# Kernel optimization log

Hardware: AMD Instinct MI355X
Metric: run time of the kernel (lower is better)

The kernel has to match this reference:

```python
import jax, jax.numpy as jnp
import numpy as np

N = 2048; K = 2048; D = 256; D_RESHAPE = 800
HA = 256; DA = 128; HK = 128; HC = 128; HS = 256
S = max(10, int(0.1 * K))  # n_sample = 204
BN_SCALE = 1.0 / float(np.sqrt(1.0 + 1e-5))  # eval BatchNorm1d with running stats (0,1)

def leaky(x):
    return jax.nn.leaky_relu(x, 0.01)

def conv2d(x, w, b):
    y = jax.lax.conv_general_dilated(x, w, (1, 1), 'VALID', dimension_numbers=('NCHW', 'OIHW', 'NCHW'))
    return y + b[None, :, None, None]

def maxpool2(x):
    return jax.lax.reduce_window(x, -jnp.inf, jax.lax.max, (1, 1, 2, 2), (1, 1, 2, 2), 'VALID')

def data_transform(x, c1w, c1b, c2w, c2b, ew, eb):
    h = maxpool2(leaky(conv2d(x, c1w, c1b)))   # [n,20,12,12]
    h = maxpool2(leaky(conv2d(h, c2w, c2b)))   # [n,50,4,4]
    h = h.reshape(-1, D_RESHAPE)
    return leaky(h @ ew.T + eb)                # [n,D]

def skip_block(X, w1, b1, w2, b2, w3, b3):
    # Conv1d kernel_size=1 == per-position linear over channels
    X1 = leaky(X @ w1.T + b1) * BN_SCALE       # [n,HC]
    X2 = leaky(X @ w2.T + b2) * BN_SCALE       # [n,HC]
    X3 = leaky(X @ w3.T + b3) * BN_SCALE       # [n,d]
    feat = jax.nn.softmax(X1 @ X2.T, axis=0)   # torch Softmax(dim=1) on [1,n,n] -> axis 0
    return feat @ X3 + X

def mask_scores(A, w1, b1, w2, b2, w3, b3, w4, b4):
    X1 = leaky(A @ w1.T + b1)                  # [n,HK]
    X2 = jnp.tanh(A @ w2.T + b2)               # [n,HK]
    M = X1.T @ X2                              # [HK,HK]
    A3 = leaky(M @ w3.T + b3)                  # [HK,K]
    s = A3.T @ w4[0] + b4[0]                   # [K]
    return jax.nn.softmax(s)

def attention(X, few, feb, vw, vb, uw, ub, aww, awb, ew, eb):
    H = leaky(X @ few.T + feb)                 # [n,HA]
    AV = jnp.tanh(H @ vw.T + vb)
    AU = leaky(H @ uw.T + ub)
    a = leaky((AV * AU) @ aww.T + awb)         # [n,1]
    A = jax.nn.softmax(a.T, axis=1)            # [1,n]
    M = leaky((A @ H) @ ew.T + eb)             # [1,d]
    return M, A

def euclid(X, Y):
    d2 = jnp.sum(X * X, 1)[:, None] + jnp.sum(Y * Y, 1)[None, :] - 2.0 * (X @ Y.T)
    return jnp.sqrt(jnp.maximum(d2, 0.0))


def setup_inputs() -> dict:
    key = jax.random.key(0)
    ks = iter(jax.random.split(key, 70))
    def rn(shape, scale=0.05):
        return jax.random.normal(next(ks), shape, dtype=jnp.float32) * scale
    d = {}
    d['B'] = jax.random.normal(next(ks), (N, 1, 28, 28), dtype=jnp.float32)
    d['KB'] = jax.random.normal(next(ks), (K, 1, 28, 28), dtype=jnp.float32)
    d['dt_c1_w'] = rn((20, 1, 5, 5)); d['dt_c1_b'] = rn((20,))
    d['dt_c2_w'] = rn((50, 20, 5, 5)); d['dt_c2_b'] = rn((50,))
    d['dt_emb_w'] = rn((D, D_RESHAPE)); d['dt_emb_b'] = rn((D,))
    for nm, dd in (('sk1', D), ('sk2', D), ('sk3', K)):
        d[nm + '_w1'] = rn((HC, dd)); d[nm + '_b1'] = rn((HC,))
        d[nm + '_w2'] = rn((HC, dd)); d[nm + '_b2'] = rn((HC,))
        d[nm + '_w3'] = rn((dd, dd)); d[nm + '_b3'] = rn((dd,))
    d['mk_w1'] = rn((HK, K)); d['mk_b1'] = rn((HK,))
    d['mk_w2'] = rn((HK, K)); d['mk_b2'] = rn((HK,))
    d['mk_w3'] = rn((K, HK)); d['mk_b3'] = rn((K,))
    d['mk_w4'] = rn((1, HK)); d['mk_b4'] = rn((1,))
    d['fuse_w'] = rn((D, D + S)); d['fuse_b'] = rn((D,))
    for nm, din in (('a1', D), ('a2', 2 * D)):
        d[nm + '_fe_w'] = rn((HA, din)); d[nm + '_fe_b'] = rn((HA,))
        d[nm + '_v_w'] = rn((DA, HA)); d[nm + '_v_b'] = rn((DA,))
        d[nm + '_u_w'] = rn((DA, HA)); d[nm + '_u_b'] = rn((DA,))
        d[nm + '_aw_w'] = rn((1, DA)); d[nm + '_aw_b'] = rn((1,))
        d[nm + '_emb_w'] = rn((din, HA)); d[nm + '_emb_b'] = rn((din,))
    d['semb_w'] = rn((HS, 2 * D)); d['semb_b'] = rn((HS,))
    d['cls_w'] = rn((1, HS)); d['cls_b'] = rn((1,))
    return d


def reference(B, KB, dt_c1_w, dt_c1_b, dt_c2_w, dt_c2_b, dt_emb_w, dt_emb_b,
              sk1_w1, sk1_b1, sk1_w2, sk1_b2, sk1_w3, sk1_b3,
              sk2_w1, sk2_b1, sk2_w2, sk2_b2, sk2_w3, sk2_b3,
              sk3_w1, sk3_b1, sk3_w2, sk3_b2, sk3_w3, sk3_b3,
              mk_w1, mk_b1, mk_w2, mk_b2, mk_w3, mk_b3, mk_w4, mk_b4,
              fuse_w, fuse_b,
              a1_fe_w, a1_fe_b, a1_v_w, a1_v_b, a1_u_w, a1_u_b, a1_aw_w, a1_aw_b, a1_emb_w, a1_emb_b,
              a2_fe_w, a2_fe_b, a2_v_w, a2_v_b, a2_u_w, a2_u_b, a2_aw_w, a2_aw_b, a2_emb_w, a2_emb_b,
              semb_w, semb_b, cls_w, cls_b):
    B_dt = data_transform(B, dt_c1_w, dt_c1_b, dt_c2_w, dt_c2_b, dt_emb_w, dt_emb_b)
    KB_dt = data_transform(KB, dt_c1_w, dt_c1_b, dt_c2_w, dt_c2_b, dt_emb_w, dt_emb_b)
    Xs = skip_block(B_dt, sk1_w1, sk1_b1, sk1_w2, sk1_b2, sk1_w3, sk1_b3)
    Ks = skip_block(KB_dt, sk2_w1, sk2_b1, sk2_w2, sk2_b2, sk2_w3, sk2_b3)
    # torch detaches the affinity (.detach().numpy())
    aff = euclid(jax.lax.stop_gradient(Xs), jax.lax.stop_gradient(Ks))  # [N,K]
    aff_s = skip_block(aff, sk3_w1, sk3_b1, sk3_w2, sk3_b2, sk3_w3, sk3_b3)
    scores = mask_scores(aff_s, mk_w1, mk_b1, mk_w2, mk_b2, mk_w3, mk_b3, mk_w4, mk_b4)
    idx = jnp.argsort(-scores)[:S]                       # top-S knowledge columns
    B_bag = jax.nn.softmax(aff_s[:, idx], axis=1)        # [N,S], torch Softmax(dim=2)
    B_fuse = leaky(jnp.concatenate([B_dt, B_bag], axis=1) @ fuse_w.T + fuse_b)  # [N,D]
    M1, _ = attention(B_fuse, a1_fe_w, a1_fe_b, a1_v_w, a1_v_b, a1_u_w, a1_u_b, a1_aw_w, a1_aw_b, a1_emb_w, a1_emb_b)
    X2 = jnp.concatenate([B_fuse, jnp.tile(M1, (B_fuse.shape[0], 1))], axis=1)  # [N,2D]
    bvec, A = attention(X2, a2_fe_w, a2_fe_b, a2_v_w, a2_v_b, a2_u_w, a2_u_b, a2_aw_w, a2_aw_b, a2_emb_w, a2_emb_b)
    bvec = leaky(bvec @ semb_w.T + semb_b)               # [1,HS]
    Y = jnp.clip(jax.nn.sigmoid(bvec @ cls_w.T + cls_b), 1e-5, 1.0 - 1e-5)
    return (Y, A)
```

## Files before the change

kernel.cpp:

```cpp
#include <hip/hip_runtime.h>
#include <math.h>

#define LEAKY(x) ((x) > 0.f ? (x) : 0.01f * (x))
static constexpr float BN_SCALE = 0.9999950000374997f;

typedef unsigned short ushort_t;
typedef float f32x4 __attribute__((ext_vector_type(4)));
typedef short bf16x8 __attribute__((ext_vector_type(8)));

__device__ __forceinline__ ushort_t f2bfu(float f) {
  union { float f; unsigned u; } v; v.f = f;
  unsigned r = v.u + 0x7fffu + ((v.u >> 16) & 1u);
  return (ushort_t)(r >> 16);
}
__device__ __forceinline__ float bfu2f(ushort_t u) {
  union { unsigned u; float f; } v; v.u = ((unsigned)u) << 16;
  return v.f;
}

__global__ void fill_out(float* out, int n) {
  int i = blockIdx.x * 256 + threadIdx.x;
  if (i < n) out[i] = 0.25f;
}

struct CvtArgs {
  const float* src[20];
  ushort_t* dst[20];
  int len[20];
};
__global__ void to_bf16_multi(CvtArgs a) {
  for (int s = 0; s < 20; ++s) {
    const float* sp = a.src[s];
    ushort_t* dp = a.dst[s];
    int n = a.len[s];
    for (int i = blockIdx.x * 256 + threadIdx.x; i < n; i += gridDim.x * 256)
      dp[i] = f2bfu(sp[i]);
  }
}

struct BiasPk { const float* a[12]; float* out; };
__global__ void bias_pack(BiasPk p) {
  int b = blockIdx.x, t = threadIdx.x;
  p.out[b * 256 + t] = (t < 128) ? p.a[2 * b][t] : p.a[2 * b + 1][t - 128];
}

__global__ void pad_fuse_bf16(const float* __restrict__ w, ushort_t* __restrict__ wp) {
  int idx = blockIdx.x * 256 + threadIdx.x;
  if (idx >= 256 * 512) return;
  int o = idx >> 9, k = idx & 511;
  wp[idx] = (k < 460) ? f2bfu(w[(size_t)o * 460 + k]) : (ushort_t)0;
}

__launch_bounds__(256)
__global__ void conv12_mfma(const float* __restrict__ imgB, const float* __restrict__ imgK,
                            const float* __restrict__ w1, const float* __restrict__ b1,
                            const ushort_t* __restrict__ w2b, const float* __restrict__ b2,
                            ushort_t* __restrict__ out800) {
  __shared__ __align__(16) char smem[39168];
  ushort_t* sh1u = (ushort_t*)smem;
  float* simg = (float*)(smem + 11520);
  float* sw1p = (float*)(smem + 18688);
  float* b1s  = (float*)(smem + 20928);
  ushort_t* As = (ushort_t*)(smem + 11520);
  ushort_t* Bs = (ushort_t*)(smem + 29952);
  float* Cf = (float*)smem;

  int tid = threadIdx.x;
  int bx = blockIdx.x;
  const float* imgb = (bx < 1024) ? imgB + (size_t)bx * 2 * 784
                                  : imgK + (size_t)(bx - 1024) * 2 * 784;

  for (int i = tid; i < 1568; i += 256) {
    int im = (i >= 784) ? 1 : 0;
    int r = i - im * 784;
    int row = r / 28, col = r - row * 28;
    int sc = col ^ ((((unsigned)row >> 1) & 1u) << 4);
    simg[im * 896 + row * 32 + sc] = imgb[i];
  }
  for (int i = tid; i < 500; i += 256) {
    int c = i / 25, tap = i - c * 25;
    sw1p[c * 28 + tap] = w1[i];
  }
  if (tid < 20) b1s[tid] = b1[tid];
  __syncthreads();

  for (int o = tid; o < 1152; o += 256) {
    int im = (o >= 576) ? 1 : 0;
    int rem = o - im * 576;
    int cg = rem / 144;
    int pos = rem - cg * 144;
    int py = pos / 12, px = pos - py * 12;
    int y0 = py * 2, x0 = px * 2;
    float p[6][6];
    #pragma unroll
    for (int yy = 0; yy < 6; ++yy) {
      int rr = y0 + yy;
      int rbase = im * 896 + rr * 32;
      int sw = (((unsigned)rr >> 1) & 1u) << 4;
      #pragma unroll
      for (int xx = 0; xx < 6; ++xx)
        p[yy][xx] = simg[rbase + ((x0 + xx) ^ sw)];
    }
    #pragma unroll
    for (int cc = 0; cc < 5; ++cc) {
      int c = cg * 5 + cc;
      float wreg[28];
      const float* wc = &sw1p[c * 28];
      #pragma unroll
      for (int q = 0; q < 7; ++q)
        *(f32x4*)&wreg[4 * q] = *(const f32x4*)(wc + 4 * q);
      float bb = b1s[c];
      float t0 = bb, t1 = bb, t2 = bb, t3 = bb;
      #pragma unroll
      for (int ky = 0; ky < 5; ++ky)
        #pragma unroll
        for (int kx = 0; kx < 5; ++kx) {
          float wv = wreg[ky * 5 + kx];
          t0 += p[ky][kx] * wv;
          t1 += p[ky][kx + 1] * wv;
          t2 += p[ky + 1][kx] * wv;
          t3 += p[ky + 1][kx + 1] * wv;
        }
      float mx = fmaxf(fmaxf(t0, t1), fmaxf(t2, t3));
      sh1u[im * 2880 + c * 144 + pos] = f2bfu(LEAKY(mx));
    }
  }

  int wave = tid >> 6, lane = tid & 63;
  int wm = (wave >> 1) * 64, wn = (wave & 1) * 32;
  int mrow = lane & 15, kq = lane >> 4;
  int kl = tid & 63, rbase = tid >> 6;

  f32x4 acc[4][2];
  #pragma unroll
  for (int i = 0; i < 4; ++i)
    #pragma unroll
    for (int j = 0; j < 2; ++j)
      #pragma unroll
      for (int r = 0; r < 4; ++r) acc[i][j][r] = 0.f;

  for (int k0 = 0; k0 < 512; k0 += 64) {
    __syncthreads();
    int k = k0 + kl;
    bool valid = k < 500;
    int ic = k / 25, tap = k - ic * 25;
    int ky = tap / 5, kx = tap - ky * 5;
    int kof = ic * 144 + ky * 12 + kx;
    ushort_t tA[32];
    #pragma unroll
    for (int i = 0; i < 32; ++i) {
      int r = rbase + 4 * i;
      int im = r >> 6, pos = r & 63, oy = pos >> 3, ox = pos & 7;
      tA[i] = valid ? sh1u[im * 2880 + kof + oy * 12 + ox] : (ushort_t)0;
    }
    ushort_t tB[16];
    #pragma unroll
    for (int i = 0; i < 16; ++i) {
      int oc = rbase + 4 * i;
      tB[i] = (valid && oc < 50) ? w2b[(size_t)oc * 500 + k] : (ushort_t)0;
    }
    #pragma unroll
    for (int i = 0; i < 32; ++i) As[(rbase + 4 * i) * 72 + kl] = tA[i];
    #pragma unroll
    for (int i = 0; i < 16; ++i) Bs[(rbase + 4 * i) * 72 + kl] = tB[i];
    __syncthreads();
    #pragma unroll
    for (int ks = 0; ks < 2; ++ks) {
      bf16x8 af[4], bf[2];
      #pragma unroll
      for (int mt = 0; mt < 4; ++mt)
        af[mt] = *(const bf16x8*)&As[(wm + mt * 16 + mrow) * 72 + ks * 32 + kq * 8];
      #pragma unroll
      for (int nt = 0; nt < 2; ++nt)
        bf[nt] = *(const bf16x8*)&Bs[(wn + nt * 16 + mrow) * 72 + ks * 32 + kq * 8];
      #pragma unroll
      for (int mt = 0; mt < 4; ++mt)
        #pragma unroll
        for (int nt = 0; nt < 2; ++nt)
          acc[mt][nt] = __builtin_amdgcn_mfma_f32_16x16x32_bf16(af[mt], bf[nt], acc[mt][nt], 0, 0, 0);
    }
  }
  __syncthreads();
  #pragma unroll
  for (int mt = 0; mt < 4; ++mt)
    #pragma unroll
    for (int nt = 0; nt < 2; ++nt) {
      int n0 = wn + nt * 16 + (lane & 15);
      #pragma unroll
      for (int r = 0; r < 4; ++r)
        Cf[(wm + mt * 16 + kq * 4 + r) * 68 + n0] = acc[mt][nt][r];
    }
  __syncthreads();
  for (int o = tid; o < 1600; o += 256) {
    int im = o / 800, oi = o - im * 800;
    int oc = oi >> 4, p = oi & 15, py = p >> 2, px = p & 3;
    int r0 = im * 64 + py * 16 + px * 2;
    float bb = b2[oc];
    float t0 = LEAKY(Cf[r0 * 68 + oc] + bb);
    float t1 = LEAKY(Cf[(r0 + 1) * 68 + oc] + bb);
    float t2 = LEAKY(Cf[(r0 + 8) * 68 + oc] + bb);
    float t3 = LEAKY(Cf[(r0 + 9) * 68 + oc] + bb);
    out800[(size_t)(bx * 2 + im) * 800 + oi] = f2bfu(fmaxf(fmaxf(t0, t1), fmaxf(t2, t3)));
  }
}

enum { EPI_NONE = 0, EPI_LEAKY = 1, EPI_LEAKY_BN = 2, EPI_TANH = 3, EPI_EUCLID = 4,
       EPI_LEAKY_BN_ROW = 5, EPI_RES = 6 };

#define LROW 40

template <int EPI>
__launch_bounds__(256)
__global__ void gemm_bf16_nt(const ushort_t* __restrict__ A, const ushort_t* __restrict__ B,
                             const float* __restrict__ bias, float* __restrict__ C32,
                             ushort_t* __restrict__ C16, int M, int N, int Kd,
                             const float* __restrict__ e1, const float* __restrict__ e2) {
  __shared__ ushort_t As[128 * LROW];
  __shared__ ushort_t Bs[128 * LROW];
  int tid = threadIdx.x;
  int bm = blockIdx.y * 128, bn = blockIdx.x * 128;
  int wave = tid >> 6, lane = tid & 63;
  int wm = (wave >> 1) * 64, wn = (wave & 1) * 64;
  int mrow = lane & 15, kq = lane >> 4;
  int srow = tid >> 1, skof = (tid & 1) * 16;

  f32x4 acc[4][4];
  #pragma unroll
  for (int i = 0; i < 4; ++i)
    #pragma unroll
    for (int j = 0; j < 4; ++j)
      #pragma unroll
      for (int r = 0; r < 4; ++r) acc[i][j][r] = 0.f;

  for (int k0 = 0; k0 < Kd; k0 += 32) {
    const uint4* ap = (const uint4*)(A + (size_t)(bm + srow) * Kd + k0 + skof);
    const uint4* bp = (const uint4*)(B + (size_t)(bn + srow) * Kd + k0 + skof);
    uint4 a0 = ap[0], a1 = ap[1];
    uint4 b0 = bp[0], b1 = bp[1];
    __syncthreads();
    *(uint4*)&As[srow * LROW + skof] = a0;
    *(uint4*)&As[srow * LROW + skof + 8] = a1;
    *(uint4*)&Bs[srow * LROW + skof] = b0;
    *(uint4*)&Bs[srow * LROW + skof + 8] = b1;
    __syncthreads();
    bf16x8 af[4], bf[4];
    #pragma unroll
    for (int mt = 0; mt < 4; ++mt)
      af[mt] = *(const bf16x8*)&As[(wm + mt * 16 + mrow) * LROW + kq * 8];
    #pragma unroll
    for (int nt = 0; nt < 4; ++nt)
      bf[nt] = *(const bf16x8*)&Bs[(wn + nt * 16 + mrow) * LROW + kq * 8];
    #pragma unroll
    for (int mt = 0; mt < 4; ++mt)
      #pragma unroll
      for (int nt = 0; nt < 4; ++nt)
        acc[mt][nt] = __builtin_amdgcn_mfma_f32_16x16x32_bf16(af[mt], bf[nt], acc[mt][nt], 0, 0, 0);
  }
  #pragma unroll
  for (int mt = 0; mt < 4; ++mt)
    #pragma unroll
    for (int nt = 0; nt < 4; ++nt) {
      int n_g = bn + wn + nt * 16 + (lane & 15);
      #pragma unroll
      for (int r = 0; r < 4; ++r) {
        int m_g = bm + wm + mt * 16 + kq * 4 + r;
        float v = acc[mt][nt][r];
        if (EPI == EPI_EUCLID) {
          v = e1[m_g] + e2[n_g] - 2.f * v;
          v = sqrtf(fmaxf(v, 0.f));
        } else if (EPI == EPI_RES) {
          v += bfu2f(((const ushort_t*)e1)[(size_t)m_g * N + n_g]);
        } else {
          if (bias) v += bias[(EPI == EPI_LEAKY_BN_ROW) ? m_g : n_g];
          if (EPI == EPI_LEAKY) v = LEAKY(v);
          else if (EPI == EPI_LEAKY_BN || EPI == EPI_LEAKY_BN_ROW) { v = LEAKY(v); v *= BN_SCALE; }
          else if (EPI == EPI_TANH) v = tanhf(v);
        }
        if (C32) C32[(size_t)m_g * N + n_g] = v;
        if (C16) C16[(size_t)m_g * N + n_g] = f2bfu(v);
      }
    }
}

__launch_bounds__(256)
__global__ void gemm_smat_z(const ushort_t* __restrict__ X12, ushort_t* __restrict__ Smat) {
  int z = blockIdx.z;
  const ushort_t* A = X12 + (size_t)z * 2048 * 256;
  const ushort_t* B = A + 128;
  ushort_t* C = Smat + (size_t)z * 2048 * 2048;
  __shared__ ushort_t As[128 * LROW];
  __shared__ ushort_t Bs[128 * LROW];
  int tid = threadIdx.x;
  int bm = blockIdx.y * 128, bn = blockIdx.x * 128;
  int wave = tid >> 6, lane = tid & 63;
  int wm = (wave >> 1) * 64, wn = (wave & 1) * 64;
  int mrow = lane & 15, kq = lane >> 4;
  int srow = tid >> 1, skof = (tid & 1) * 16;

  f32x4 acc[4][4];
  #pragma unroll
  for (int i = 0; i < 4; ++i)
    #pragma unroll
    for (int j = 0; j < 4; ++j)
      #pragma unroll
      for (int r = 0; r < 4; ++r) acc[i][j][r] = 0.f;

  for (int k0 = 0; k0 < 128; k0 += 32) {
    const uint4* ap = (const uint4*)(A + (size_t)(bm + srow) * 256 + k0 + skof);
    const uint4* bp = (const uint4*)(B + (size_t)(bn + srow) * 256 + k0 + skof);
    uint4 a0 = ap[0], a1 = ap[1];
    uint4 b0 = bp[0], b1 = bp[1];
    __syncthreads();
    *(uint4*)&As[srow * LROW + skof] = a0;
    *(uint4*)&As[srow * LROW + skof + 8] = a1;
    *(uint4*)&Bs[srow * LROW + skof] = b0;
    *(uint4*)&Bs[srow * LROW + skof + 8] = b1;
    __syncthreads();
    bf16x8 af[4], bf[4];
    #pragma unroll
    for (int mt = 0; mt < 4; ++mt)
      af[mt] = *(const bf16x8*)&As[(wm + mt * 16 + mrow) * LROW + kq * 8];
    #pragma unroll
    for (int nt = 0; nt < 4; ++nt)
      bf[nt] = *(const bf16x8*)&Bs[(wn + nt * 16 + mrow) * LROW + kq * 8];
    #pragma unroll
    for (int mt = 0; mt < 4; ++mt)
      #pragma unroll
      for (int nt = 0; nt < 4; ++nt)
        acc[mt][nt] = __builtin_amdgcn_mfma_f32_16x16x32_bf16(af[mt], bf[nt], acc[mt][nt], 0, 0, 0);
  }
  #pragma unroll
  for (int mt = 0; mt < 4; ++mt)
    #pragma unroll
    for (int nt = 0; nt < 4; ++nt) {
      int n_g = bn + wn + nt * 16 + (lane & 15);
      #pragma unroll
      for (int r = 0; r < 4; ++r) {
        int m_g = bm + wm + mt * 16 + kq * 4 + r;
        C[(size_t)m_g * 2048 + n_g] = f2bfu(acc[mt][nt][r]);
      }
    }
}

template <int EPI>
__launch_bounds__(256)
__global__ void gemm_bf16_nt64(const ushort_t* __restrict__ A, const ushort_t* __restrict__ B,
                               const float* __restrict__ bias, float* __restrict__ C32,
                               ushort_t* __restrict__ C16, int M, int N, int Kd) {
  __shared__ ushort_t As[64 * LROW];
  __shared__ ushort_t Bs[64 * LROW];
  int tid = threadIdx.x;
  int bm = blockIdx.y * 64, bn = blockIdx.x * 64;
  int wave = tid >> 6, lane = tid & 63;
  int wm = (wave >> 1) * 32, wn = (wave & 1) * 32;
  int mrow = lane & 15, kq = lane >> 4;
  int srow = tid >> 2, skof = (tid & 3) * 8;

  f32x4 acc[2][2];
  #pragma unroll
  for (int i = 0; i < 2; ++i)
    #pragma unroll
    for (int j = 0; j < 2; ++j)
      #pragma unroll
      for (int r = 0; r < 4; ++r) acc[i][j][r] = 0.f;

  for (int k0 = 0; k0 < Kd; k0 += 32) {
    uint4 a0 = *(const uint4*)(A + (size_t)(bm + srow) * Kd + k0 + skof);
    uint4 b0 = *(const uint4*)(B + (size_t)(bn + srow) * Kd + k0 + skof);
    __syncthreads();
    *(uint4*)&As[srow * LROW + skof] = a0;
    *(uint4*)&Bs[srow * LROW + skof] = b0;
    __syncthreads();
    bf16x8 af[2], bf[2];
    #pragma unroll
    for (int mt = 0; mt < 2; ++mt)
      af[mt] = *(const bf16x8*)&As[(wm + mt * 16 + mrow) * LROW + kq * 8];
    #pragma unroll
    for (int nt = 0; nt < 2; ++nt)
      bf[nt] = *(const bf16x8*)&Bs[(wn + nt * 16 + mrow) * LROW + kq * 8];
    #pragma unroll
    for (int mt = 0; mt < 2; ++mt)
      #pragma unroll
      for (int nt = 0; nt < 2; ++nt)
        acc[mt][nt] = __builtin_amdgcn_mfma_f32_16x16x32_bf16(af[mt], bf[nt], acc[mt][nt], 0, 0, 0);
  }
  #pragma unroll
  for (int mt = 0; mt < 2; ++mt)
    #pragma unroll
    for (int nt = 0; nt < 2; ++nt) {
      int n_g = bn + wn + nt * 16 + (lane & 15);
      #pragma unroll
      for (int r = 0; r < 4; ++r) {
        int m_g = bm + wm + mt * 16 + kq * 4 + r;
        float v = acc[mt][nt][r];
        if (bias) v += bias[n_g];
        if (EPI == EPI_LEAKY) v = LEAKY(v);
        else if (EPI == EPI_LEAKY_BN) { v = LEAKY(v); v *= BN_SCALE; }
        else if (EPI == EPI_TANH) v = tanhf(v);
        if (C32) C32[(size_t)m_g * N + n_g] = v;
        if (C16) C16[(size_t)m_g * N + n_g] = f2bfu(v);
      }
    }
}

template <int EPI>
__launch_bounds__(256)
__global__ void gemm_nt64_dual(const ushort_t* __restrict__ A, const ushort_t* __restrict__ B1,
                               const ushort_t* __restrict__ B2, const float* __restrict__ bias1,
                               const float* __restrict__ bias2, ushort_t* __restrict__ C16,
                               int M, int N, int Kd, int Msplit) {
  __shared__ ushort_t As[64 * LROW];
  __shared__ ushort_t Bs[64 * LROW];
  int tid = threadIdx.x;
  int bm = blockIdx.y * 64, bn = blockIdx.x * 64;
  const ushort_t* B = (bm < Msplit) ? B1 : B2;
  const float* bias = (bm < Msplit) ? bias1 : bias2;
  int wave = tid >> 6, lane = tid & 63;
  int wm = (wave >> 1) * 32, wn = (wave & 1) * 32;
  int mrow = lane & 15, kq = lane >> 4;
  int srow = tid >> 2, skof = (tid & 3) * 8;

  f32x4 acc[2][2];
  #pragma unroll
  for (int i = 0; i < 2; ++i)
    #pragma unroll
    for (int j = 0; j < 2; ++j)
      #pragma unroll
      for (int r = 0; r < 4; ++r) acc[i][j][r] = 0.f;

  for (int k0 = 0; k0 < Kd; k0 += 32) {
    uint4 a0 = *(const uint4*)(A + (size_t)(bm + srow) * Kd + k0 + skof);
    uint4 b0 = *(const uint4*)(B + (size_t)(bn + srow) * Kd + k0 + skof);
    __syncthreads();
    *(uint4*)&As[srow * LROW + skof] = a0;
    *(uint4*)&Bs[srow * LROW + skof] = b0;
    __syncthreads();
    bf16x8 af[2], bf[2];
    #pragma unroll
    for (int mt = 0; mt < 2; ++mt)
      af[mt] = *(const bf16x8*)&As[(wm + mt * 16 + mrow) * LROW + kq * 8];
    #pragma unroll
    for (int nt = 0; nt < 2; ++nt)
      bf[nt] = *(const bf16x8*)&Bs[(wn + nt * 16 + mrow) * LROW + kq * 8];
    #pragma unroll
    for (int mt = 0; mt < 2; ++mt)
      #pragma unroll
      for (int nt = 0; nt < 2; ++nt)
        acc[mt][nt] = __builtin_amdgcn_mfma_f32_16x16x32_bf16(af[mt], bf[nt], acc[mt][nt], 0, 0, 0);
  }
  #pragma unroll
  for (int mt = 0; mt < 2; ++mt)
    #pragma unroll
    for (int nt = 0; nt < 2; ++nt) {
      int n_g = bn + wn + nt * 16 + (lane & 15);
      #pragma unroll
      for (int r = 0; r < 4; ++r) {
        int m_g = bm + wm + mt * 16 + kq * 4 + r;
        float v = acc[mt][nt][r] + bias[n_g];
        if (EPI == EPI_LEAKY) v = LEAKY(v);
        else if (EPI == EPI_LEAKY_BN) { v = LEAKY(v); v *= BN_SCALE; }
        C16[(size_t)m_g * N + n_g] = f2bfu(v);
      }
    }
}

template <int EPI1, int EPI2>
__launch_bounds__(256)
__global__ void gemm_nt64_split(const ushort_t* __restrict__ A, const ushort_t* __restrict__ B,
                                const float* __restrict__ biasPk, float* __restrict__ C32,
                                ushort_t* __restrict__ C16, int M, int N, int Kd, int Nsplit) {
  __shared__ ushort_t As[64 * LROW];
  __shared__ ushort_t Bs[64 * LROW];
  int tid = threadIdx.x;
  int bm = blockIdx.y * 64, bn = blockIdx.x * 64;
  int wave = tid >> 6, lane = tid & 63;
  int wm = (wave >> 1) * 32, wn = (wave & 1) * 32;
  int mrow = lane & 15, kq = lane >> 4;
  int srow = tid >> 2, skof = (tid & 3) * 8;

  f32x4 acc[2][2];
  #pragma unroll
  for (int i = 0; i < 2; ++i)
    #pragma unroll
    for (int j = 0; j < 2; ++j)
      #pragma unroll
      for (int r = 0; r < 4; ++r) acc[i][j][r] = 0.f;

  for (int k0 = 0; k0 < Kd; k0 += 32) {
    uint4 a0 = *(const uint4*)(A + (size_t)(bm + srow) * Kd + k0 + skof);
    uint4 b0 = *(const uint4*)(B + (size_t)(bn + srow) * Kd + k0 + skof);
    __syncthreads();
    *(uint4*)&As[srow * LROW + skof] = a0;
    *(uint4*)&Bs[srow * LROW + skof] = b0;
    __syncthreads();
    bf16x8 af[2], bf[2];
    #pragma unroll
    for (int mt = 0; mt < 2; ++mt)
      af[mt] = *(const bf16x8*)&As[(wm + mt * 16 + mrow) * LROW + kq * 8];
    #pragma unroll
    for (int nt = 0; nt < 2; ++nt)
      bf[nt] = *(const bf16x8*)&Bs[(wn + nt * 16 + mrow) * LROW + kq * 8];
    #pragma unroll
    for (int mt = 0; mt < 2; ++mt)
      #pragma unroll
      for (int nt = 0; nt < 2; ++nt)
        acc[mt][nt] = __builtin_amdgcn_mfma_f32_16x16x32_bf16(af[mt], bf[nt], acc[mt][nt], 0, 0, 0);
  }
  #pragma unroll
  for (int mt = 0; mt < 2; ++mt)
    #pragma unroll
    for (int nt = 0; nt < 2; ++nt) {
      int n_g = bn + wn + nt * 16 + (lane & 15);
      #pragma unroll
      for (int r = 0; r < 4; ++r) {
        int m_g = bm + wm + mt * 16 + kq * 4 + r;
        float v = acc[mt][nt][r] + biasPk[n_g];
        if (n_g < Nsplit) {
          if (EPI1 == EPI_LEAKY) v = LEAKY(v);
          else if (EPI1 == EPI_TANH) v = tanhf(v);
        } else {
          if (EPI2 == EPI_LEAKY) v = LEAKY(v);
          else if (EPI2 == EPI_TANH) v = tanhf(v);
        }
        if (C32) C32[(size_t)m_g * N + n_g] = v;
        if (C16) C16[(size_t)m_g * N + n_g] = f2bfu(v);
      }
    }
}

__launch_bounds__(256)
__global__ void gemm_w3T_z(const ushort_t* __restrict__ W3a, const ushort_t* __restrict__ W3b,
                           const float* __restrict__ b3a, const float* __restrict__ b3b,
                           const ushort_t* __restrict__ dtb, ushort_t* __restrict__ X3T) {
  const int N = 2048, Kd = 256;
  int z = blockIdx.z;
  const ushort_t* A = z ? W3b : W3a;
  const float* bias = z ? b3b : b3a;
  const ushort_t* B = dtb + (size_t)z * 2048 * 256;
  ushort_t* C = X3T + (size_t)z * 256 * 2048;
  __shared__ ushort_t As[64 * LROW];
  __shared__ ushort_t Bs[64 * LROW];
  int tid = threadIdx.x;
  int bm = blockIdx.y * 64, bn = blockIdx.x * 64;
  int wave = tid >> 6, lane = tid & 63;
  int wm = (wave >> 1) * 32, wn = (wave & 1) * 32;
  int mrow = lane & 15, kq = lane >> 4;
  int srow = tid >> 2, skof = (tid & 3) * 8;

  f32x4 acc[2][2];
  #pragma unroll
  for (int i = 0; i < 2; ++i)
    #pragma unroll
    for (int j = 0; j < 2; ++j)
      #pragma unroll
      for (int r = 0; r < 4; ++r) acc[i][j][r] = 0.f;

  for (int k0 = 0; k0 < Kd; k0 += 32) {
    uint4 a0 = *(const uint4*)(A + (size_t)(bm + srow) * Kd + k0 + skof);
    uint4 b0 = *(const uint4*)(B + (size_t)(bn + srow) * Kd + k0 + skof);
    __syncthreads();
    *(uint4*)&As[srow * LROW + skof] = a0;
    *(uint4*)&Bs[srow * LROW + skof] = b0;
    __syncthreads();
    bf16x8 af[2], bf[2];
    #pragma unroll
    for (int mt = 0; mt < 2; ++mt)
      af[mt] = *(const bf16x8*)&As[(wm + mt * 16 + mrow) * LROW + kq * 8];
    #pragma unroll
    for (int nt = 0; nt < 2; ++nt)
      bf[nt] = *(const bf16x8*)&Bs[(wn + nt * 16 + mrow) * LROW + kq * 8];
    #pragma unroll
    for (int mt = 0; mt < 2; ++mt)
      #pragma unroll
      for (int nt = 0; nt < 2; ++nt)
        acc[mt][nt] = __builtin_amdgcn_mfma_f32_16x16x32_bf16(af[mt], bf[nt], acc[mt][nt], 0, 0, 0);
  }
  #pragma unroll
  for (int mt = 0; mt < 2; ++mt)
    #pragma unroll
    for (int nt = 0; nt < 2; ++nt) {
      int n_g = bn + wn + nt * 16 + (lane & 15);
      #pragma unroll
      for (int r = 0; r < 4; ++r) {
        int m_g = bm + wm + mt * 16 + kq * 4 + r;
        float v = acc[mt][nt][r] + bias[m_g];
        v = LEAKY(v); v *= BN_SCALE;
        C[(size_t)m_g * N + n_g] = f2bfu(v);
      }
    }
}

__launch_bounds__(256)
__global__ void gemm_ntt_res64_z(const ushort_t* __restrict__ SmatBase,
                                 const ushort_t* __restrict__ X3T,
                                 const ushort_t* __restrict__ dtb,
                                 ushort_t* __restrict__ XsKs) {
  const int N = 256, Kd = 2048;
  int z = blockIdx.z;
  const ushort_t* A = SmatBase + (size_t)z * 2048 * 2048;
  const ushort_t* B = X3T + (size_t)z * 256 * 2048;
  const ushort_t* R = dtb + (size_t)z * 2048 * 256;
  ushort_t* C = XsKs + (size_t)z * 2048 * 256;
  __shared__ ushort_t As[64 * LROW];
  __shared__ ushort_t Bs[64 * LROW];
  int tid = threadIdx.x;
  int bm = blockIdx.y * 64, bn = blockIdx.x * 64;
  int wave = tid >> 6, lane = tid & 63;
  int wm = (wave >> 1) * 32, wn = (wave & 1) * 32;
  int mrow = lane & 15, kq = lane >> 4;
  int srow = tid >> 2, skof = (tid & 3) * 8;

  f32x4 acc[2][2];
  #pragma unroll
  for (int i = 0; i < 2; ++i)
    #pragma unroll
    for (int j = 0; j < 2; ++j)
      #pragma unroll
      for (int r = 0; r < 4; ++r) acc[i][j][r] = 0.f;

  for (int k0 = 0; k0 < Kd; k0 += 32) {
    uint4 a0 = *(const uint4*)(A + (size_t)(bm + srow) * Kd + k0 + skof);
    uint4 b0 = *(const uint4*)(B + (size_t)(bn + srow) * Kd + k0 + skof);
    __syncthreads();
    *(uint4*)&As[srow * LROW + skof] = a0;
    *(uint4*)&Bs[srow * LROW + skof] = b0;
    __syncthreads();
    bf16x8 af[2], bf[2];
    #pragma unroll
    for (int mt = 0; mt < 2; ++mt)
      af[mt] = *(const bf16x8*)&As[(wm + mt * 16 + mrow) * LROW + kq * 8];
    #pragma unroll
    for (int nt = 0; nt < 2; ++nt)
      bf[nt] = *(const bf16x8*)&Bs[(wn + nt * 16 + mrow) * LROW + kq * 8];
    #pragma unroll
    for (int mt = 0; mt < 2; ++mt)
      #pragma unroll
      for (int nt = 0; nt < 2; ++nt)
        acc[mt][nt] = __builtin_amdgcn_mfma_f32_16x16x32_bf16(af[mt], bf[nt], acc[mt][nt], 0, 0, 0);
  }
  #pragma unroll
  for (int mt = 0; mt < 2; ++mt)
    #pragma unroll
    for (int nt = 0; nt < 2; ++nt) {
      int n_g = bn + wn + nt * 16 + (lane & 15);
      #pragma unroll
      for (int r = 0; r < 4; ++r) {
        int m_g = bm + wm + mt * 16 + kq * 4 + r;
        float v = acc[mt][nt][r] + bfu2f(R[(size_t)m_g * N + n_g]);
        C[(size_t)m_g * N + n_g] = f2bfu(v);
      }
    }
}

__global__ void gemm_tn_part(const ushort_t* __restrict__ X, float* __restrict__ part) {
  int tx = threadIdx.x & 15, ty = threadIdx.x >> 4;
  int i = blockIdx.y * 16 + ty, j = blockIdx.x * 16 + tx;
  int ks = blockIdx.z;
  float acc = 0.f;
  for (int k = ks * 128; k < ks * 128 + 128; ++k)
    acc += bfu2f(X[(size_t)k * 256 + i]) * bfu2f(X[(size_t)k * 256 + 128 + j]);
  part[(size_t)ks * 16384 + i * 128 + j] = acc;
}
__global__ void gemm_tn_reduce(const float* __restrict__ part, ushort_t* __restrict__ Mm) {
  int idx = blockIdx.x * 256 + threadIdx.x;
  float s = 0.f;
  #pragma unroll
  for (int ks = 0; ks < 16; ++ks) s += part[(size_t)ks * 16384 + idx];
  Mm[idx] = f2bfu(s);
}

__global__ void smax_partA(const ushort_t* __restrict__ Sb, float* __restrict__ pm,
                           float* __restrict__ pl, int N) {
  int z = blockIdx.z;
  const ushort_t* S = Sb + (size_t)z * 2048 * 2048;
  int t = threadIdx.x;
  int col = blockIdx.x * 64 + (t & 63);
  int g = t >> 6;
  int r0 = blockIdx.y * 128 + g;
  float vals[32];
  #pragma unroll
  for (int i = 0; i < 32; ++i)
    vals[i] = bfu2f(S[(size_t)(r0 + 4 * i) * N + col]);
  float m = -1e30f;
  #pragma unroll
  for (int i = 0; i < 32; ++i) m = fmaxf(m, vals[i]);
  float l = 0.f;
  #pragma unroll
  for (int i = 0; i < 32; ++i) l += expf(vals[i] - m);
  __shared__ float rm[4][64], rl[4][64];
  rm[g][t & 63] = m; rl[g][t & 63] = l;
  __syncthreads();
  if (g == 0) {
    int c = t & 63;
    float M0 = rm[0][c], L0 = rl[0][c];
    #pragma unroll
    for (int j = 1; j < 4; ++j) {
      float Mj = rm[j][c], Lj = rl[j][c];
      float nm = fmaxf(M0, Mj);
      L0 = L0 * expf(M0 - nm) + Lj * expf(Mj - nm);
      M0 = nm;
    }
    pm[((size_t)z * 16 + blockIdx.y) * N + col] = M0;
    pl[((size_t)z * 16 + blockIdx.y) * N + col] = L0;
  }
}
__global__ void smax_partB(const float* __restrict__ pm, const float* __restrict__ pl,
                           float* __restrict__ gm, float* __restrict__ gi, int N) {
  int z = blockIdx.y;
  int col = blockIdx.x * 256 + threadIdx.x;
  float m = -1e30f, l = 0.f;
  for (int b = 0; b < 16; ++b) {
    float bm = pm[((size_t)z * 16 + b) * N + col], bl = pl[((size_t)z * 16 + b) * N + col];
    float nm = fmaxf(m, bm);
    l = l * expf(m - nm) + bl * expf(bm - nm);
    m = nm;
  }
  gm[(size_t)z * N + col] = m;
  gi[(size_t)z * N + col] = 1.f / l;
}
__global__ void smax_partC(ushort_t* __restrict__ Sb, const float* __restrict__ gm,
                           const float* __restrict__ gi, int N) {
  int z = blockIdx.z;
  ushort_t* S = Sb + (size_t)z * 2048 * 2048;
  int t = threadIdx.x;
  int col = blockIdx.x * 64 + (t & 63);
  int g = t >> 6;
  float m = gm[(size_t)z * N + col], inv = gi[(size_t)z * N + col];
  int r0 = blockIdx.y * 128 + g;
  #pragma unroll 8
  for (int i = 0; i < 32; ++i) {
    size_t idx = (size_t)(r0 + 4 * i) * N + col;
    S[idx] = f2bfu(expf(bfu2f(S[idx]) - m) * inv);
  }
}

__global__ void row_norm_bf16(const ushort_t* __restrict__ X, float* __restrict__ out, int Kd) {
  int r = blockIdx.x;
  int t = threadIdx.x;
  float s = 0.f;
  for (int k = t; k < Kd; k += 64) { float v = bfu2f(X[(size_t)r * Kd + k]); s += v * v; }
  for (int off = 32; off; off >>= 1) s += __shfl_down(s, off);
  if (t == 0) out[r] = s;
}

__global__ void mask_score(const float* __restrict__ A3, const float* __restrict__ w4,
                           const float* __restrict__ b4, float* __restrict__ s) {
  int k = blockIdx.x * 256 + threadIdx.x;
  float acc = b4[0];
  for (int h = 0; h < 128; ++h) acc += A3[(size_t)h * 2048 + k] * w4[h];
  s[k] = acc;
}

__global__ void topk_rank(const float* __restrict__ s, int* __restrict__ idx, int K, int S) {
  __shared__ float sv[2048];
  int t = threadIdx.x;
  for (int i = t; i < K; i += 256) sv[i] = s[i];
  __syncthreads();
  int j = blockIdx.x * 256 + t;
  if (j >= K) return;
  float sj = sv[j];
  int rank = 0;
  #pragma unroll 8
  for (int i = 0; i < 2048; ++i) {
    float si = sv[i];
    rank += (si > sj) || (si == sj && i < j);
  }
  if (rank < S) idx[rank] = j;
}

__global__ void build_cat(const ushort_t* __restrict__ Bdt, const ushort_t* __restrict__ affs,
                          const int* __restrict__ idx, ushort_t* __restrict__ cat) {
  int r = blockIdx.x, t = threadIdx.x;
  __shared__ float vals[256];
  __shared__ float red[256];
  float v = -1e30f;
  if (t < 204) {
    int ix = idx[t];
    ix = ix < 0 ? 0 : (ix > 2047 ? 2047 : ix);
    v = bfu2f(affs[(size_t)r * 2048 + ix]);
  }
  vals[t] = v;
  red[t] = v;
  __syncthreads();
  for (int off = 128; off; off >>= 1) { if (t < off) red[t] = fmaxf(red[t], red[t + off]); __syncthreads(); }
  float m = red[0];
  __syncthreads();
// ... 270 lines not shown
```

Before: 922.5 us.

## Use direct global-to-LDS loads in all bf16 GEMM kernels, simplify conv1 staging

```diff
diff --git a/kernel.cpp b/kernel.cpp
--- a/kernel.cpp
+++ b/kernel.cpp
@@ -16,6 +16,12 @@
 __device__ __forceinline__ float bfu2f(ushort_t u) {
   union { unsigned u; float f; } v; v.u = ((unsigned)u) << 16;
   return v.f;
+}
+
+__device__ __forceinline__ void gload16(const ushort_t* g, ushort_t* lds) {
+  __builtin_amdgcn_global_load_lds(
+      (const __attribute__((address_space(1))) void*)g,
+      (__attribute__((address_space(3))) void*)lds, 16, 0, 0);
 }
 
 __global__ void fill_out(float* out, int n) {
@@ -59,7 +65,7 @@
   __shared__ __align__(16) char smem[39168];
   ushort_t* sh1u = (ushort_t*)smem;
   float* simg = (float*)(smem + 11520);
-  float* sw1p = (float*)(smem + 18688);
+  float* sw1  = (float*)(smem + 18688);
   float* b1s  = (float*)(smem + 20928);
   ushort_t* As = (ushort_t*)(smem + 11520);
   ushort_t* Bs = (ushort_t*)(smem + 29952);
@@ -74,13 +80,10 @@
     int im = (i >= 784) ? 1 : 0;
     int r = i - im * 784;
     int row = r / 28, col = r - row * 28;
-    int sc = col ^ ((((unsigned)row >> 1) & 1u) << 4);
+    int sc = (col + (row >> 1)) & 31;
     simg[im * 896 + row * 32 + sc] = imgb[i];
   }
-  for (int i = tid; i < 500; i += 256) {
-    int c = i / 25, tap = i - c * 25;
-    sw1p[c * 28 + tap] = w1[i];
-  }
+  for (int i = tid; i < 500; i += 256) sw1[i] = w1[i];
   if (tid < 20) b1s[tid] = b1[tid];
   __syncthreads();
 
@@ -96,26 +99,22 @@
     for (int yy = 0; yy < 6; ++yy) {
       int rr = y0 + yy;
       int rbase = im * 896 + rr * 32;
-      int sw = (((unsigned)rr >> 1) & 1u) << 4;
+      int rot = rr >> 1;
       #pragma unroll
       for (int xx = 0; xx < 6; ++xx)
-        p[yy][xx] = simg[rbase + ((x0 + xx) ^ sw)];
+        p[yy][xx] = simg[rbase + ((x0 + xx + rot) & 31)];
     }
     #pragma unroll
     for (int cc = 0; cc < 5; ++cc) {
       int c = cg * 5 + cc;
-      float wreg[28];
-      const float* wc = &sw1p[c * 28];
-      #pragma unroll
-      for (int q = 0; q < 7; ++q)
-        *(f32x4*)&wreg[4 * q] = *(const f32x4*)(wc + 4 * q);
+      const float* wc = &sw1[c * 25];
       float bb = b1s[c];
       float t0 = bb, t1 = bb, t2 = bb, t3 = bb;
       #pragma unroll
       for (int ky = 0; ky < 5; ++ky)
         #pragma unroll
         for (int kx = 0; kx < 5; ++kx) {
-          float wv = wreg[ky * 5 + kx];
+          float wv = wc[ky * 5 + kx];
           t0 += p[ky][kx] * wv;
           t1 += p[ky][kx + 1] * wv;
           t2 += p[ky + 1][kx] * wv;
@@ -215,14 +214,18 @@
                              const float* __restrict__ bias, float* __restrict__ C32,
                              ushort_t* __restrict__ C16, int M, int N, int Kd,
                              const float* __restrict__ e1, const float* __restrict__ e2) {
-  __shared__ ushort_t As[128 * LROW];
-  __shared__ ushort_t Bs[128 * LROW];
+  __shared__ __align__(16) ushort_t As[128 * 32];
+  __shared__ __align__(16) ushort_t Bs[128 * 32];
   int tid = threadIdx.x;
   int bm = blockIdx.y * 128, bn = blockIdx.x * 128;
   int wave = tid >> 6, lane = tid & 63;
   int wm = (wave >> 1) * 64, wn = (wave & 1) * 64;
   int mrow = lane & 15, kq = lane >> 4;
-  int srow = tid >> 1, skof = (tid & 1) * 16;
+  int l0 = tid, l1 = tid + 256;
+  const ushort_t* ga0 = A + (size_t)(bm + (l0 >> 2)) * Kd + (l0 & 3) * 8;
+  const ushort_t* ga1 = A + (size_t)(bm + (l1 >> 2)) * Kd + (l1 & 3) * 8;
+  const ushort_t* gb0 = B + (size_t)(bn + (l0 >> 2)) * Kd + (l0 & 3) * 8;
+  const ushort_t* gb1 = B + (size_t)(bn + (l1 >> 2)) * Kd + (l1 & 3) * 8;
 
   f32x4 acc[4][4];
   #pragma unroll
@@ -233,23 +236,19 @@
       for (int r = 0; r < 4; ++r) acc[i][j][r] = 0.f;
 
   for (int k0 = 0; k0 < Kd; k0 += 32) {
-    const uint4* ap = (const uint4*)(A + (size_t)(bm + srow) * Kd + k0 + skof);
-    const uint4* bp = (const uint4*)(B + (size_t)(bn + srow) * Kd + k0 + skof);
-    uint4 a0 = ap[0], a1 = ap[1];
-    uint4 b0 = bp[0], b1 = bp[1];
-    __syncthreads();
-    *(uint4*)&As[srow * LROW + skof] = a0;
-    *(uint4*)&As[srow * LROW + skof + 8] = a1;
-    *(uint4*)&Bs[srow * LROW + skof] = b0;
-    *(uint4*)&Bs[srow * LROW + skof + 8] = b1;
+    __syncthreads();
+    gload16(ga0 + k0, &As[l0 * 8]);
+    gload16(ga1 + k0, &As[l1 * 8]);
+    gload16(gb0 + k0, &Bs[l0 * 8]);
+    gload16(gb1 + k0, &Bs[l1 * 8]);
     __syncthreads();
     bf16x8 af[4], bf[4];
     #pragma unroll
     for (int mt = 0; mt < 4; ++mt)
-      af[mt] = *(const bf16x8*)&As[(wm + mt * 16 + mrow) * LROW + kq * 8];
+      af[mt] = *(const bf16x8*)&As[(wm + mt * 16 + mrow) * 32 + kq * 8];
     #pragma unroll
     for (int nt = 0; nt < 4; ++nt)
-      bf[nt] = *(const bf16x8*)&Bs[(wn + nt * 16 + mrow) * LROW + kq * 8];
+      bf[nt] = *(const bf16x8*)&Bs[(wn + nt * 16 + mrow) * 32 + kq * 8];
     #pragma unroll
     for (int mt = 0; mt < 4; ++mt)
       #pragma unroll
@@ -288,14 +287,18 @@
   const ushort_t* A = X12 + (size_t)z * 2048 * 256;
   const ushort_t* B = A + 128;
   ushort_t* C = Smat + (size_t)z * 2048 * 2048;
-  __shared__ ushort_t As[128 * LROW];
-  __shared__ ushort_t Bs[128 * LROW];
+  __shared__ __align__(16) ushort_t As[128 * 32];
+  __shared__ __align__(16) ushort_t Bs[128 * 32];
   int tid = threadIdx.x;
   int bm = blockIdx.y * 128, bn = blockIdx.x * 128;
   int wave = tid >> 6, lane = tid & 63;
   int wm = (wave >> 1) * 64, wn = (wave & 1) * 64;
   int mrow = lane & 15, kq = lane >> 4;
-  int srow = tid >> 1, skof = (tid & 1) * 16;
+  int l0 = tid, l1 = tid + 256;
+  const ushort_t* ga0 = A + (size_t)(bm + (l0 >> 2)) * 256 + (l0 & 3) * 8;
+  const ushort_t* ga1 = A + (size_t)(bm + (l1 >> 2)) * 256 + (l1 & 3) * 8;
+  const ushort_t* gb0 = B + (size_t)(bn + (l0 >> 2)) * 256 + (l0 & 3) * 8;
+  const ushort_t* gb1 = B + (size_t)(bn + (l1 >> 2)) * 256 + (l1 & 3) * 8;
 
   f32x4 acc[4][4];
   #pragma unroll
@@ -306,23 +309,19 @@
       for (int r = 0; r < 4; ++r) acc[i][j][r] = 0.f;
 
   for (int k0 = 0; k0 < 128; k0 += 32) {
-    const uint4* ap = (const uint4*)(A + (size_t)(bm + srow) * 256 + k0 + skof);
-    const uint4* bp = (const uint4*)(B + (size_t)(bn + srow) * 256 + k0 + skof);
-    uint4 a0 = ap[0], a1 = ap[1];
-    uint4 b0 = bp[0], b1 = bp[1];
-    __syncthreads();
-    *(uint4*)&As[srow * LROW + skof] = a0;
-    *(uint4*)&As[srow * LROW + skof + 8] = a1;
-    *(uint4*)&Bs[srow * LROW + skof] = b0;
-    *(uint4*)&Bs[srow * LROW + skof + 8] = b1;
+    __syncthreads();
+    gload16(ga0 + k0, &As[l0 * 8]);
+    gload16(ga1 + k0, &As[l1 * 8]);
+    gload16(gb0 + k0, &Bs[l0 * 8]);
+    gload16(gb1 + k0, &Bs[l1 * 8]);
     __syncthreads();
     bf16x8 af[4], bf[4];
     #pragma unroll
     for (int mt = 0; mt < 4; ++mt)
-      af[mt] = *(const bf16x8*)&As[(wm + mt * 16 + mrow) * LROW + kq * 8];
+      af[mt] = *(const bf16x8*)&As[(wm + mt * 16 + mrow) * 32 + kq * 8];
     #pragma unroll
     for (int nt = 0; nt < 4; ++nt)
-      bf[nt] = *(const bf16x8*)&Bs[(wn + nt * 16 + mrow) * LROW + kq * 8];
+      bf[nt] = *(const bf16x8*)&Bs[(wn + nt * 16 + mrow) * 32 + kq * 8];
     #pragma unroll
     for (int mt = 0; mt < 4; ++mt)
       #pragma unroll
@@ -347,14 +346,15 @@
 __global__ void gemm_bf16_nt64(const ushort_t* __restrict__ A, const ushort_t* __restrict__ B,
                                const float* __restrict__ bias, float* __restrict__ C32,
                                ushort_t* __restrict__ C16, int M, int N, int Kd) {
-  __shared__ ushort_t As[64 * LROW];
-  __shared__ ushort_t Bs[64 * LROW];
+  __shared__ __align__(16) ushort_t As[64 * 32];
+  __shared__ __align__(16) ushort_t Bs[64 * 32];
   int tid = threadIdx.x;
   int bm = blockIdx.y * 64, bn = blockIdx.x * 64;
   int wave = tid >> 6, lane = tid & 63;
   int wm = (wave >> 1) * 32, wn = (wave & 1) * 32;
   int mrow = lane & 15, kq = lane >> 4;
-  int srow = tid >> 2, skof = (tid & 3) * 8;
+  const ushort_t* ga = A + (size_t)(bm + (tid >> 2)) * Kd + (tid & 3) * 8;
+  const ushort_t* gb = B + (size_t)(bn + (tid >> 2)) * Kd + (tid & 3) * 8;
 
   f32x4 acc[2][2];
   #pragma unroll
@@ -365,19 +365,17 @@
       for (int r = 0; r < 4; ++r) acc[i][j][r] = 0.f;
 
   for (int k0 = 0; k0 < Kd; k0 += 32) {
-    uint4 a0 = *(const uint4*)(A + (size_t)(bm + srow) * Kd + k0 + skof);
-    uint4 b0 = *(const uint4*)(B + (size_t)(bn + srow) * Kd + k0 + skof);
-    __syncthreads();
-    *(uint4*)&As[srow * LROW + skof] = a0;
-    *(uint4*)&Bs[srow * LROW + skof] = b0;
+    __syncthreads();
+    gload16(ga + k0, &As[tid * 8]);
+    gload16(gb + k0, &Bs[tid * 8]);
     __syncthreads();
     bf16x8 af[2], bf[2];
     #pragma unroll
     for (int mt = 0; mt < 2; ++mt)
-      af[mt] = *(const bf16x8*)&As[(wm + mt * 16 + mrow) * LROW + kq * 8];
+      af[mt] = *(const bf16x8*)&As[(wm + mt * 16 + mrow) * 32 + kq * 8];
     #pragma unroll
     for (int nt = 0; nt < 2; ++nt)
-      bf[nt] = *(const bf16x8*)&Bs[(wn + nt * 16 + mrow) * LROW + kq * 8];
+      bf[nt] = *(const bf16x8*)&Bs[(wn + nt * 16 + mrow) * 32 + kq * 8];
     #pragma unroll
     for (int mt = 0; mt < 2; ++mt)
       #pragma unroll
@@ -409,8 +407,8 @@
                                const ushort_t* __restrict__ B2, const float* __restrict__ bias1,
                                const float* __restrict__ bias2, ushort_t* __restrict__ C16,
                                int M, int N, int Kd, int Msplit) {
-  __shared__ ushort_t As[64 * LROW];
-  __shared__ ushort_t Bs[64 * LROW];
+  __shared__ __align__(16) ushort_t As[64 * 32];
+  __shared__ __align__(16) ushort_t Bs[64 * 32];
   int tid = threadIdx.x;
   int bm = blockIdx.y * 64, bn = blockIdx.x * 64;
   const ushort_t* B = (bm < Msplit) ? B1 : B2;
@@ -418,7 +416,8 @@
   int wave = tid >> 6, lane = tid & 63;
   int wm = (wave >> 1) * 32, wn = (wave & 1) * 32;
   int mrow = lane & 15, kq = lane >> 4;
-  int srow = tid >> 2, skof = (tid & 3) * 8;
+  const ushort_t* ga = A + (size_t)(bm + (tid >> 2)) * Kd + (tid & 3) * 8;
+  const ushort_t* gb = B + (size_t)(bn + (tid >> 2)) * Kd + (tid & 3) * 8;
 
   f32x4 acc[2][2];
   #pragma unroll
@@ -429,19 +428,17 @@
       for (int r = 0; r < 4; ++r) acc[i][j][r] = 0.f;
 
   for (int k0 = 0; k0 < Kd; k0 += 32) {
-    uint4 a0 = *(const uint4*)(A + (size_t)(bm + srow) * Kd + k0 + skof);
-    uint4 b0 = *(const uint4*)(B + (size_t)(bn + srow) * Kd + k0 + skof);
-    __syncthreads();
-    *(uint4*)&As[srow * LROW + skof] = a0;
-    *(uint4*)&Bs[srow * LROW + skof] = b0;
+    __syncthreads();
+    gload16(ga + k0, &As[tid * 8]);
+    gload16(gb + k0, &Bs[tid * 8]);
     __syncthreads();
     bf16x8 af[2], bf[2];
     #pragma unroll
     for (int mt = 0; mt < 2; ++mt)
-      af[mt] = *(const bf16x8*)&As[(wm + mt * 16 + mrow) * LROW + kq * 8];
+      af[mt] = *(const bf16x8*)&As[(wm + mt * 16 + mrow) * 32 + kq * 8];
     #pragma unroll
     for (int nt = 0; nt < 2; ++nt)
-      bf[nt] = *(const bf16x8*)&Bs[(wn + nt * 16 + mrow) * LROW + kq * 8];
+      bf[nt] = *(const bf16x8*)&Bs[(wn + nt * 16 + mrow) * 32 + kq * 8];
     #pragma unroll
     for (int mt = 0; mt < 2; ++mt)
       #pragma unroll
@@ -469,14 +466,15 @@
 __global__ void gemm_nt64_split(const ushort_t* __restrict__ A, const ushort_t* __restrict__ B,
                                 const float* __restrict__ biasPk, float* __restrict__ C32,
                                 ushort_t* __restrict__ C16, int M, int N, int Kd, int Nsplit) {
-  __shared__ ushort_t As[64 * LROW];
-  __shared__ ushort_t Bs[64 * LROW];
+  __shared__ __align__(16) ushort_t As[64 * 32];
+  __shared__ __align__(16) ushort_t Bs[64 * 32];
   int tid = threadIdx.x;
   int bm = blockIdx.y * 64, bn = blockIdx.x * 64;
   int wave = tid >> 6, lane = tid & 63;
   int wm = (wave >> 1) * 32, wn = (wave & 1) * 32;
   int mrow = lane & 15, kq = lane >> 4;
-  int srow = tid >> 2, skof = (tid & 3) * 8;
+  const ushort_t* ga = A + (size_t)(bm + (tid >> 2)) * Kd + (tid & 3) * 8;
+  const ushort_t* gb = B + (size_t)(bn + (tid >> 2)) * Kd + (tid & 3) * 8;
 
   f32x4 acc[2][2];
   #pragma unroll
@@ -487,19 +485,17 @@
       for (int r = 0; r < 4; ++r) acc[i][j][r] = 0.f;
 
   for (int k0 = 0; k0 < Kd; k0 += 32) {
-    uint4 a0 = *(const uint4*)(A + (size_t)(bm + srow) * Kd + k0 + skof);
-    uint4 b0 = *(const uint4*)(B + (size_t)(bn + srow) * Kd + k0 + skof);
-    __syncthreads();
-    *(uint4*)&As[srow * LROW + skof] = a0;
-    *(uint4*)&Bs[srow * LROW + skof] = b0;
+    __syncthreads();
+    gload16(ga + k0, &As[tid * 8]);
+    gload16(gb + k0, &Bs[tid * 8]);
     __syncthreads();
     bf16x8 af[2], bf[2];
     #pragma unroll
     for (int mt = 0; mt < 2; ++mt)
-      af[mt] = *(const bf16x8*)&As[(wm + mt * 16 + mrow) * LROW + kq * 8];
+      af[mt] = *(const bf16x8*)&As[(wm + mt * 16 + mrow) * 32 + kq * 8];
     #pragma unroll
     for (int nt = 0; nt < 2; ++nt)
-      bf[nt] = *(const bf16x8*)&Bs[(wn + nt * 16 + mrow) * LROW + kq * 8];
+      bf[nt] = *(const bf16x8*)&Bs[(wn + nt * 16 + mrow) * 32 + kq * 8];
     #pragma unroll
     for (int mt = 0; mt < 2; ++mt)
       #pragma unroll
@@ -538,14 +534,15 @@
   const float* bias = z ? b3b : b3a;
   const ushort_t* B = dtb + (size_t)z * 2048 * 256;
   ushort_t* C = X3T + (size_t)z * 256 * 2048;
-  __shared__ ushort_t As[64 * LROW];
-  __shared__ ushort_t Bs[64 * LROW];
+  __shared__ __align__(16) ushort_t As[64 * 32];
+  __shared__ __align__(16) ushort_t Bs[64 * 32];
   int tid = threadIdx.x;
   int bm = blockIdx.y * 64, bn = blockIdx.x * 64;
   int wave = tid >> 6, lane = tid & 63;
   int wm = (wave >> 1) * 32, wn = (wave & 1) * 32;
   int mrow = lane & 15, kq = lane >> 4;
-  int srow = tid >> 2, skof = (tid & 3) * 8;
+  const ushort_t* ga = A + (size_t)(bm + (tid >> 2)) * Kd + (tid & 3) * 8;
+  const ushort_t* gb = B + (size_t)(bn + (tid >> 2)) * Kd + (tid & 3) * 8;
 
   f32x4 acc[2][2];
   #pragma unroll
@@ -556,19 +553,17 @@
       for (int r = 0; r < 4; ++r) acc[i][j][r] = 0.f;
 
   for (int k0 = 0; k0 < Kd; k0 += 32) {
-    uint4 a0 = *(const uint4*)(A + (size_t)(bm + srow) * Kd + k0 + skof);
-    uint4 b0 = *(const uint4*)(B + (size_t)(bn + srow) * Kd + k0 + skof);
-    __syncthreads();
-    *(uint4*)&As[srow * LROW + skof] = a0;
-    *(uint4*)&Bs[srow * LROW + skof] = b0;
+    __syncthreads();
+    gload16(ga + k0, &As[tid * 8]);
+    gload16(gb + k0, &Bs[tid * 8]);
     __syncthreads();
     bf16x8 af[2], bf[2];
     #pragma unroll
     for (int mt = 0; mt < 2; ++mt)
-      af[mt] = *(const bf16x8*)&As[(wm + mt * 16 + mrow) * LROW + kq * 8];
+      af[mt] = *(const bf16x8*)&As[(wm + mt * 16 + mrow) * 32 + kq * 8];
     #pragma unroll
     for (int nt = 0; nt < 2; ++nt)
-      bf[nt] = *(const bf16x8*)&Bs[(wn + nt * 16 + mrow) * LROW + kq * 8];
+      bf[nt] = *(const bf16x8*)&Bs[(wn + nt * 16 + mrow) * 32 + kq * 8];
     #pragma unroll
     for (int mt = 0; mt < 2; ++mt)
       #pragma unroll
@@ -601,14 +596,15 @@
   const ushort_t* B = X3T + (size_t)z * 256 * 2048;
   const ushort_t* R = dtb + (size_t)z * 2048 * 256;
   ushort_t* C = XsKs + (size_t)z * 2048 * 256;
-  __shared__ ushort_t As[64 * LROW];
-  __shared__ ushort_t Bs[64 * LROW];
+  __shared__ __align__(16) ushort_t As[64 * 32];
+  __shared__ __align__(16) ushort_t Bs[64 * 32];
   int tid = threadIdx.x;
   int bm = blockIdx.y * 64, bn = blockIdx.x * 64;
   int wave = tid >> 6, lane = tid & 63;
   int wm = (wave >> 1) * 32, wn = (wave & 1) * 32;
   int mrow = lane & 15, kq = lane >> 4;
-  int srow = tid >> 2, skof = (tid & 3) * 8;
+  const ushort_t* ga = A + (size_t)(bm + (tid >> 2)) * Kd + (tid & 3) * 8;
+  const ushort_t* gb = B + (size_t)(bn + (tid >> 2)) * Kd + (tid & 3) * 8;
 
   f32x4 acc[2][2];
   #pragma unroll
@@ -619,19 +615,17 @@
       for (int r = 0; r < 4; ++r) acc[i][j][r] = 0.f;
 
   for (int k0 = 0; k0 < Kd; k0 += 32) {
-    uint4 a0 = *(const uint4*)(A + (size_t)(bm + srow) * Kd + k0 + skof);
-    uint4 b0 = *(const uint4*)(B + (size_t)(bn + srow) * Kd + k0 + skof);
-    __syncthreads();
-    *(uint4*)&As[srow * LROW + skof] = a0;
-    *(uint4*)&Bs[srow * LROW + skof] = b0;
+    __syncthreads();
+    gload16(ga + k0, &As[tid * 8]);
+    gload16(gb + k0, &Bs[tid * 8]);
     __syncthreads();
     bf16x8 af[2], bf[2];
     #pragma unroll
     for (int mt = 0; mt < 2; ++mt)
-      af[mt] = *(const bf16x8*)&As[(wm + mt * 16 + mrow) * LROW + kq * 8];
+      af[mt] = *(const bf16x8*)&As[(wm + mt * 16 + mrow) * 32 + kq * 8];
     #pragma unroll
     for (int nt = 0; nt < 2; ++nt)
-      bf[nt] = *(const bf16x8*)&Bs[(wn + nt * 16 + mrow) * LROW + kq * 8];
+      bf[nt] = *(const bf16x8*)&Bs[(wn + nt * 16 + mrow) * 32 + kq * 8];
     #pragma unroll
     for (int mt = 0; mt < 2; ++mt)
       #pragma unroll
```

After: 911.3 us. About the same (-1.2%).
